# Kernel optimization log

Hardware: AMD Instinct MI355X
Metric: run time of the kernel (lower is better)

Reference implementation:

```python
import jax, jax.numpy as jnp
import numpy as np

ALPHA, GAMMA = 0.25, 2.0
CLASS_W, COORD_W, MASK_W = 2.0, 5.0, 5.0
EPS = 1e-8


def point_sample(masks, coords):
    """Bilinear sample (grid_sample, align_corners=False, zero padding).
    masks: [R, H, W]; coords: [P, 2] as (x, y) in [0, 1]. Returns [R, P]."""
    H, W = masks.shape[-2:]
    gx = 2.0 * coords[:, 0] - 1.0
    gy = 2.0 * coords[:, 1] - 1.0
    x = ((gx + 1.0) * W - 1.0) * 0.5
    y = ((gy + 1.0) * H - 1.0) * 0.5
    x0 = jnp.floor(x)
    y0 = jnp.floor(y)
    wx1 = x - x0
    wy1 = y - y0
    wx0 = 1.0 - wx1
    wy0 = 1.0 - wy1
    x0i = x0.astype(jnp.int32)
    y0i = y0.astype(jnp.int32)
    x1i = x0i + 1
    y1i = y0i + 1

    def gather(ix, iy):
        valid = ((ix >= 0) & (ix < W) & (iy >= 0) & (iy < H)).astype(masks.dtype)
        ixc = jnp.clip(ix, 0, W - 1)
        iyc = jnp.clip(iy, 0, H - 1)
        return masks[:, iyc, ixc] * valid  # [R, P]

    return (gather(x0i, y0i) * (wx0 * wy0)
            + gather(x1i, y0i) * (wx1 * wy0)
            + gather(x0i, y1i) * (wx0 * wy1)
            + gather(x1i, y1i) * (wx1 * wy1))


def setup_inputs() -> dict:
    key = jax.random.key(0)
    k1, k2, k3, k4, k5, k6 = jax.random.split(key, 6)
    bs, Q, n_ctrl, Hm, Wm, T, P = 8, 300, 16, 128, 128, 160, 12544
    return {
        "pred_logits": jax.random.normal(k1, (bs, Q, 1), jnp.float32),
        "pred_ctrl_points": jax.random.uniform(k2, (bs, Q, n_ctrl, 2), jnp.float32),
        "pred_seg_mask": jax.random.normal(k3, (bs, Q, Hm, Wm), jnp.float32),
        "tgt_pts": jax.random.uniform(k4, (T, n_ctrl, 2), jnp.float32),
        "tgt_masks": jax.random.uniform(k5, (T, Hm, Wm), jnp.float32),
        "point_coords": jax.random.uniform(k6, (P, 2), jnp.float32),
        "lvl": 0,
    }


def reference(pred_logits, pred_ctrl_points, pred_seg_mask, tgt_pts, tgt_masks, point_coords, lvl):
    bs, Q = pred_logits.shape[:2]
    out_prob = jax.nn.sigmoid(pred_logits.reshape(bs * Q, -1))          # [N, 1]
    out_pts = pred_ctrl_points.reshape(bs * Q, -1)                      # [N, 2*n_ctrl]
    tgt_flat = tgt_pts.reshape(tgt_pts.shape[0], -1)                    # [T, 2*n_ctrl]

    cost_mask_dice = 0.0
    if lvl < 2:  # num_seg_layers
        out_masks = pred_seg_mask.reshape(bs * Q, *pred_seg_mask.shape[-2:])
        # nearest-interp of tgt_masks to out_masks size is identity (same size)
        t_pts_samp = point_sample(tgt_masks, point_coords)              # [T, P]
        o_pts_samp = point_sample(out_masks, point_coords)              # [N, P]
        s = jax.nn.sigmoid(o_pts_samp)                                  # dice_loss sigmoids inputs
        numerator = 2.0 * jnp.einsum('np,tp->nt', s, t_pts_samp)        # [N, T]
        denominator = s.sum(-1)[:, None] + t_pts_samp.sum(-1)[None, :]
        cost_mask_dice = 1.0 - (numerator + 1.0) / (denominator + 1.0)

    neg_cost = (1.0 - ALPHA) * out_prob ** GAMMA * (-jnp.log(1.0 - out_prob + EPS))
    pos_cost = ALPHA * (1.0 - out_prob) ** GAMMA * (-jnp.log(out_prob + EPS))
    cost_class = pos_cost - neg_cost                                    # [N, 1]

    cost_kpts = jnp.abs(out_pts[:, None, :] - tgt_flat[None, :, :]).sum(-1)  # L1 cdist [N, T]

    C = CLASS_W * cost_class + COORD_W * cost_kpts + MASK_W * cost_mask_dice
    return C.reshape(bs, Q, -1)
```

## Files before the change

### kernel.cpp

```cpp
#include <hip/hip_runtime.h>
#include <hip/hip_bf16.h>
#include <cstdint>

#define HW 128
#define MASK_ELEMS (HW * HW)
#define SBLK 1024
#define NBLK 256

typedef unsigned short ushort_t;
typedef __attribute__((ext_vector_type(4))) unsigned short ushort4_t;
typedef __attribute__((ext_vector_type(8))) short short8;
typedef __attribute__((ext_vector_type(4))) float f32x4;

__device__ __forceinline__ float asf(unsigned int u) {
    union { unsigned int i; float f; } c;
    c.i = u;
    return c.f;
}
__device__ __forceinline__ ushort_t f2bf(float f) {
    union { float f; unsigned int i; } c;
    c.f = f;
    unsigned int r = c.i + 0x7FFFu + ((c.i >> 16) & 1u);
    return (ushort_t)(r >> 16);
}

__global__ void kprep(const float* __restrict__ coords, int* __restrict__ idx,
                      uint2* __restrict__ wpk, int P) {
    int i = blockIdx.x * 256 + threadIdx.x;
    if (i >= P) return;
    float cx = coords[2 * i], cy = coords[2 * i + 1];
    float x = cx * (float)HW - 0.5f;
    float y = cy * (float)HW - 0.5f;
    float x0f = floorf(x), y0f = floorf(y);
    float wx1 = x - x0f, wy1 = y - y0f;
    float wx0 = 1.f - wx1, wy0 = 1.f - wy1;
    int x0 = (int)x0f, y0 = (int)y0f;

    float wxA = (x0 >= 0) ? wx0 : wx1;
    float wxB = (x0 >= 0 && x0 < HW - 1) ? wx1 : 0.f;
    float wyA = (y0 >= 0) ? wy0 : wy1;
    float wyB = (y0 >= 0 && y0 < HW - 1) ? wy1 : 0.f;
    int bx = max(x0, 0), by = max(y0, 0);
    if (bx > HW - 2) { bx = HW - 2; wxB = wxA; wxA = 0.f; }
    if (by > HW - 2) { by = HW - 2; wyB = wyA; wyA = 0.f; }

    idx[i] = by * HW + bx;
    wpk[i] = make_uint2((unsigned)f2bf(wxA * wyA) | ((unsigned)f2bf(wxB * wyA) << 16),
                        (unsigned)f2bf(wxA * wyB) | ((unsigned)f2bf(wxB * wyB) << 16));
}

__device__ __forceinline__ void stage_mask(const float* __restrict__ g, float* l, int tid) {
    #pragma unroll
    for (int j = 0; j < MASK_ELEMS / (SBLK * 4); ++j) {
        int o = j * SBLK * 4 + tid * 4;
        __builtin_amdgcn_global_load_lds(
            (const __attribute__((address_space(1))) unsigned int*)(const void*)(g + o),
            (__attribute__((address_space(3))) unsigned int*)(void*)(l + o), 16, 0, 0);
    }
}

__global__ __launch_bounds__(SBLK) void ksamp_all(
        const float* __restrict__ pmask, const float* __restrict__ tmasks,
        const int* __restrict__ idx, const uint2* __restrict__ wpk,
        ushort_t* __restrict__ S, ushort_t* __restrict__ tsamp,
        float* __restrict__ ssum, float* __restrict__ tsum,
        const int* __restrict__ lvl, int N, int T, int P) {
    if (*lvl >= 2) return;
    __shared__ float buf[2][MASK_ELEMS];
    __shared__ float wred[2][SBLK / 64];
    __shared__ int4  tmi[64];
    __shared__ uint4 tma[64], tmb[64];
    const int tid = threadIdx.x;
    const int NM = N + T;
    const int nq = P >> 2;
    const int ntail = nq - 3 * SBLK;

    int4 idr[3];
    uint4 war[3], wbr[3];
    #pragma unroll
    for (int it = 0; it < 3; ++it) {
        int q = it * SBLK + tid;
        if (q < nq) {
            idr[it] = ((const int4*)idx)[q];
            war[it] = ((const uint4*)wpk)[2 * q];
            wbr[it] = ((const uint4*)wpk)[2 * q + 1];
        } else {
            idr[it] = make_int4(0, 0, 0, 0);
            war[it] = make_uint4(0, 0, 0, 0);
            wbr[it] = make_uint4(0, 0, 0, 0);
        }
    }

    auto mptr = [&](int mi) -> const float* {
        return (mi < N) ? pmask + (size_t)mi * MASK_ELEMS
                        : tmasks + (size_t)(mi - N) * MASK_ELEMS;
    };

    const int b = blockIdx.x;
    const int rounds = (NM - b + NBLK - 1) / NBLK;
    if (rounds <= 0) return;

    stage_mask(mptr(b), buf[0], tid);
    if (ntail > 0 && ntail <= 64 && tid < ntail) {
        int q = 3 * SBLK + tid;
        tmi[tid] = ((const int4*)idx)[q];
        tma[tid] = ((const uint4*)wpk)[2 * q];
        tmb[tid] = ((const uint4*)wpk)[2 * q + 1];
    }
    asm volatile("s_waitcnt vmcnt(0)" ::: "memory");
    asm volatile("s_waitcnt lgkmcnt(0)" ::: "memory");
    __builtin_amdgcn_s_barrier();

    int cur = 0;
    for (int k = 0; k < rounds; ++k) {
        if (k + 1 < rounds)
            stage_mask(mptr(b + (k + 1) * NBLK), buf[cur ^ 1], tid);

        const float* lm = buf[cur];
        const int mi = b + k * NBLK;
        const bool sig = (mi < N);
        ushort4_t* o4 = sig ? (ushort4_t*)(S + (size_t)mi * P)
                            : (ushort4_t*)(tsamp + (size_t)(mi - N) * P);
        float sum = 0.f;

        auto do_quad = [&](int4 id, uint4 wa4, uint4 wb4, int q) {
            float v[4];
            int bi[4] = {id.x, id.y, id.z, id.w};
            unsigned wa[4] = {wa4.x, wa4.z, wb4.x, wb4.z};
            unsigned wb[4] = {wa4.y, wa4.w, wb4.y, wb4.w};
            #pragma unroll
            for (int p2 = 0; p2 < 4; ++p2) {
                int bb = bi[p2];
                float t00 = lm[bb], t01 = lm[bb + 1];
                float t10 = lm[bb + HW], t11 = lm[bb + HW + 1];
                float vv = asf(wa[p2] << 16) * t00 + asf(wa[p2] & 0xffff0000u) * t01
                         + asf(wb[p2] << 16) * t10 + asf(wb[p2] & 0xffff0000u) * t11;
                if (sig) vv = __builtin_amdgcn_rcpf(1.f + __expf(-vv));
                v[p2] = vv;
            }
            ushort4_t o = {f2bf(v[0]), f2bf(v[1]), f2bf(v[2]), f2bf(v[3])};
            o4[q] = o;
            sum += (v[0] + v[1]) + (v[2] + v[3]);
        };

        #pragma unroll
        for (int it = 0; it < 3; ++it) {
            int q = it * SBLK + tid;
            if (q < nq) do_quad(idr[it], war[it], wbr[it], q);
        }
        if (ntail > 0 && ntail <= 64) {
            int tq = tid >> 4;
            if (((tid & 15) == 0) && tq < ntail)
                do_quad(tmi[tq], tma[tq], tmb[tq], 3 * SBLK + tq);
        } else if (ntail > 64) {
            for (int q = 3 * SBLK + tid; q < nq; q += SBLK)
                do_quad(((const int4*)idx)[q], ((const uint4*)wpk)[2 * q],
                        ((const uint4*)wpk)[2 * q + 1], q);
        }

        #pragma unroll
        for (int m2 = 32; m2 > 0; m2 >>= 1) sum += __shfl_xor(sum, m2, 64);
        if ((tid & 63) == 0) wred[k & 1][tid >> 6] = sum;
        asm volatile("s_waitcnt vmcnt(0)" ::: "memory");
        asm volatile("s_waitcnt lgkmcnt(0)" ::: "memory");
        __builtin_amdgcn_s_barrier();
        if (tid == 0) {
            float s = 0.f;
            #pragma unroll
            for (int w2 = 0; w2 < SBLK / 64; ++w2) s += wred[k & 1][w2];
            if (sig) ssum[mi] = s;
            else tsum[mi - N] = s;
        }
        cur ^= 1;
    }
}

#define LDF(Aarr, Barr, kof)                                                              \
    do {                                                                                  \
        _Pragma("unroll") for (int m_ = 0; m_ < 3; ++m_)                                  \
            Aarr[m_] = *(const short8*)(pa + (size_t)m_ * 16 * P + (kof));                \
        _Pragma("unroll") for (int j_ = 0; j_ < 5; ++j_)                                  \
            Barr[j_] = *(const short8*)(pb + (size_t)j_ * 16 * P + (kof));                \
    } while (0)

#define FMAS(Aarr, Barr)                                                                  \
    do {                                                                                  \
        _Pragma("unroll") for (int m_ = 0; m_ < 3; ++m_) {                                \
            _Pragma("unroll") for (int j_ = 0; j_ < 5; ++j_)                              \
                acc[m_][j_] = __builtin_amdgcn_mfma_f32_16x16x32_bf16(                    \
                    Aarr[m_], Barr[j_], acc[m_][j_], 0, 0, 0);                            \
        }                                                                                 \
    } while (0)

__global__ __launch_bounds__(256) void kgemm(const ushort_t* __restrict__ S,
                                             const ushort_t* __restrict__ Tm,
                                             float* __restrict__ Cpart,
                                             const int* __restrict__ lvl,
                                             int N, int T, int P, int nsteps) {
    if (*lvl >= 2) return;
    int tid = threadIdx.x;
    int wid = tid >> 6, lane = tid & 63;
    int wm = wid >> 1, wt = wid & 1;
    int r = lane & 15, g = lane >> 4;
    int n0 = blockIdx.x * 96 + wm * 48;
    int t0 = wt * 80;
    size_t k0 = (size_t)blockIdx.y * nsteps * 32 + g * 8;
    const ushort_t* pa = S + (size_t)(n0 + r) * P + k0;
    const ushort_t* pb = Tm + (size_t)(t0 + r) * P + k0;

    f32x4 acc[3][5];
    #pragma unroll
    for (int m2 = 0; m2 < 3; ++m2)
        #pragma unroll
        for (int j2 = 0; j2 < 5; ++j2) acc[m2][j2] = (f32x4){0.f, 0.f, 0.f, 0.f};

    short8 a0[3], b0[5], a1[3], b1[5];
    LDF(a0, b0, 0);
    int ks = 0;
    for (; ks + 2 < nsteps; ks += 2) {
        LDF(a1, b1, (ks + 1) * 32);
        FMAS(a0, b0);
        LDF(a0, b0, (ks + 2) * 32);
        FMAS(a1, b1);
    }
    LDF(a1, b1, (ks + 1) * 32);
    FMAS(a0, b0);
    FMAS(a1, b1);

    size_t cb = (size_t)blockIdx.y * N * T;
    #pragma unroll
    for (int m2 = 0; m2 < 3; ++m2)
        #pragma unroll
        for (int j2 = 0; j2 < 5; ++j2)
            #pragma unroll
            for (int q = 0; q < 4; ++q) {
                int row = n0 + m2 * 16 + g * 4 + q;
                int col = t0 + j2 * 16 + r;
                Cpart[cb + (size_t)row * T + col] = acc[m2][j2][q];
            }
}

__global__ void kfinal(const float* __restrict__ logits, const float* __restrict__ opts,
                       const float* __restrict__ tpts, const float* __restrict__ Cpart,
                       const float* __restrict__ ssum, const float* __restrict__ tsum,
                       const int* __restrict__ lvl, float* __restrict__ out,
                       int N, int T, int nks) {
    int idx = blockIdx.x * 256 + threadIdx.x;
    if (idx >= N * T) return;
    int n = idx / T, t = idx - n * T;

    float lg = logits[n];
    float p = 1.f / (1.f + __expf(-lg));
    float pos = 0.25f * (1.f - p) * (1.f - p) * (-logf(p + 1e-8f));
    float neg = 0.75f * p * p * (-logf(1.f - p + 1e-8f));
    float ccls = pos - neg;

    float kp = 0.f;
    const float4* a4 = (const float4*)(opts + (size_t)n * 32);
    const float4* b4 = (const float4*)(tpts + (size_t)t * 32);
    #pragma unroll
    for (int j = 0; j < 8; ++j) {
        float4 a = a4[j], b = b4[j];
        kp += fabsf(a.x - b.x) + fabsf(a.y - b.y) + fabsf(a.z - b.z) + fabsf(a.w - b.w);
    }

    float dice = 0.f;
    if (*lvl < 2) {
        float dot = 0.f;
        for (int ks = 0; ks < nks; ++ks) dot += Cpart[(size_t)ks * N * T + idx];
        dice = 1.f - (2.f * dot + 1.f) / (ssum[n] + tsum[t] + 1.f);
    }
    out[idx] = 2.f * ccls + 5.f * kp + 5.f * dice;
}

extern "C" void kernel_launch(void* const* d_in, const int* in_sizes, int n_in,
                              void* d_out, int out_size, void* d_ws, size_t ws_size,
                              hipStream_t stream) {
    const float* logits = (const float*)d_in[0];
    const float* cpts   = (const float*)d_in[1];
    const float* pmask  = (const float*)d_in[2];
    const float* tpts   = (const float*)d_in[3];
    const float* tmasks = (const float*)d_in[4];
    const float* coords = (const float*)d_in[5];
    const int*   lvl    = (const int*)d_in[6];
    float* out = (float*)d_out;

    int N = in_sizes[0];
    int T = in_sizes[3] / 32;
    int P = in_sizes[5] / 2;

    char* w = (char*)d_ws;
    auto alloc = [&](size_t bytes) {
        char* r = w;
        w += (bytes + 255) & ~(size_t)255;
        return r;
    };
    int*      idxb  = (int*)alloc((size_t)P * 4);
    uint2*    wpkb  = (uint2*)alloc((size_t)P * 8);
    ushort_t* tsamp = (ushort_t*)alloc((size_t)T * P * 2);
    ushort_t* S     = (ushort_t*)alloc((size_t)N * P * 2);
    float*    ssumb = (float*)alloc((size_t)N * 4);
    float*    tsumb = (float*)alloc((size_t)T * 4);
    size_t base_bytes = (size_t)(w - (char*)d_ws);

    int nks = 14;
    if (base_bytes + (size_t)nks * N * T * 4 > ws_size) nks = 7;
    int nsteps = (P / 32) / nks;
    float* Cpart = (float*)alloc((size_t)nks * N * T * 4);

    kprep<<<(P + 255) / 256, 256, 0, stream>>>(coords, idxb, wpkb, P);
    ksamp_all<<<NBLK, SBLK, 0, stream>>>(pmask, tmasks, idxb, wpkb, S, tsamp,
                                         ssumb, tsumb, lvl, N, T, P);
    kgemm<<<dim3(N / 96, nks), 256, 0, stream>>>(S, tsamp, Cpart, lvl, N, T, P, nsteps);
    kfinal<<<(N * T + 255) / 256, 256, 0, stream>>>(logits, cpts, tpts, Cpart, ssumb, tsumb,
                                                    lvl, out, N, T, nks);
}
```

Measured before the change: 129.8 us.

## Warp-specialize sampling kernel into loader and sampler waves with LDS flag sync

Splits the 1024-thread block into 4 producer waves that copy each mask from global into a double-buffered LDS slot via registers, and 12 consumer waves that bilinear-sample it. The two groups synchronize through LDS atomic counters with spin-waits instead of block-wide barriers. The aim is to overlap mask staging with sampling and remove per-round full barriers. In exchange it drops the async global_load_lds path and the register-cached indices/weights, reloading them every round. Spin-waiting also consumes issue slots and carries hang risk, bounded only by a guard counter.

```diff
diff --git a/kernel.cpp b/kernel.cpp
--- a/kernel.cpp
+++ b/kernel.cpp
@@ -6,6 +6,10 @@
 #define MASK_ELEMS (HW * HW)
 #define SBLK 1024
 #define NBLK 256
+#define NSW 12
+#define NLW 4
+#define STH (NSW * 64)
+#define LTH (NLW * 64)
 
 typedef unsigned short ushort_t;
 typedef __attribute__((ext_vector_type(4))) unsigned short ushort4_t;
@@ -22,6 +26,15 @@
     c.f = f;
     unsigned int r = c.i + 0x7FFFu + ((c.i >> 16) & 1u);
     return (ushort_t)(r >> 16);
+}
+
+__device__ __forceinline__ void spin_ge(int* p, int target) {
+    int guard = 0;
+    while (__hip_atomic_load(p, __ATOMIC_ACQUIRE, __HIP_MEMORY_SCOPE_WORKGROUP) < target) {
+        __builtin_amdgcn_s_sleep(1);
+        if (++guard > (1 << 28)) break;
+    }
+    __builtin_amdgcn_sched_barrier(0);
 }
 
 __global__ void kprep(const float* __restrict__ coords, int* __restrict__ idx,
@@ -49,16 +62,6 @@
                         (unsigned)f2bf(wxA * wyB) | ((unsigned)f2bf(wxB * wyB) << 16));
 }
 
-__device__ __forceinline__ void stage_mask(const float* __restrict__ g, float* l, int tid) {
-    #pragma unroll
-    for (int j = 0; j < MASK_ELEMS / (SBLK * 4); ++j) {
-        int o = j * SBLK * 4 + tid * 4;
-        __builtin_amdgcn_global_load_lds(
-            (const __attribute__((address_space(1))) unsigned int*)(const void*)(g + o),
-            (__attribute__((address_space(3))) unsigned int*)(void*)(l + o), 16, 0, 0);
-    }
-}
-
 __global__ __launch_bounds__(SBLK) void ksamp_all(
         const float* __restrict__ pmask, const float* __restrict__ tmasks,
         const int* __restrict__ idx, const uint2* __restrict__ wpk,
@@ -67,111 +70,105 @@
         const int* __restrict__ lvl, int N, int T, int P) {
     if (*lvl >= 2) return;
     __shared__ float buf[2][MASK_ELEMS];
-    __shared__ float wred[2][SBLK / 64];
-    __shared__ int4  tmi[64];
-    __shared__ uint4 tma[64], tmb[64];
+    __shared__ float wred[4][NSW];
+    __shared__ int part_cnt, cons_cnt;
     const int tid = threadIdx.x;
+    const int wid = tid >> 6, lane = tid & 63;
     const int NM = N + T;
     const int nq = P >> 2;
-    const int ntail = nq - 3 * SBLK;
-
-    int4 idr[3];
-    uint4 war[3], wbr[3];
-    #pragma unroll
-    for (int it = 0; it < 3; ++it) {
-        int q = it * SBLK + tid;
-        if (q < nq) {
-            idr[it] = ((const int4*)idx)[q];
-            war[it] = ((const uint4*)wpk)[2 * q];
-            wbr[it] = ((const uint4*)wpk)[2 * q + 1];
-        } else {
-            idr[it] = make_int4(0, 0, 0, 0);
-            war[it] = make_uint4(0, 0, 0, 0);
-            wbr[it] = make_uint4(0, 0, 0, 0);
-        }
-    }
+
+    if (tid == 0) { part_cnt = 0; cons_cnt = 0; }
+    __syncthreads();
+
+    const int b = blockIdx.x;
+    const int rounds = (NM - b + NBLK - 1) / NBLK;
+    if (rounds <= 0) return;
 
     auto mptr = [&](int mi) -> const float* {
         return (mi < N) ? pmask + (size_t)mi * MASK_ELEMS
                         : tmasks + (size_t)(mi - N) * MASK_ELEMS;
     };
 
-    const int b = blockIdx.x;
-    const int rounds = (NM - b + NBLK - 1) / NBLK;
-    if (rounds <= 0) return;
-
-    stage_mask(mptr(b), buf[0], tid);
-    if (ntail > 0 && ntail <= 64 && tid < ntail) {
-        int q = 3 * SBLK + tid;
-        tmi[tid] = ((const int4*)idx)[q];
-        tma[tid] = ((const uint4*)wpk)[2 * q];
-        tmb[tid] = ((const uint4*)wpk)[2 * q + 1];
-    }
-    asm volatile("s_waitcnt vmcnt(0)" ::: "memory");
-    asm volatile("s_waitcnt lgkmcnt(0)" ::: "memory");
-    __builtin_amdgcn_s_barrier();
-
-    int cur = 0;
-    for (int k = 0; k < rounds; ++k) {
-        if (k + 1 < rounds)
-            stage_mask(mptr(b + (k + 1) * NBLK), buf[cur ^ 1], tid);
-
-        const float* lm = buf[cur];
-        const int mi = b + k * NBLK;
-        const bool sig = (mi < N);
-        ushort4_t* o4 = sig ? (ushort4_t*)(S + (size_t)mi * P)
-                            : (ushort4_t*)(tsamp + (size_t)(mi - N) * P);
-        float sum = 0.f;
-
-        auto do_quad = [&](int4 id, uint4 wa4, uint4 wb4, int q) {
-            float v[4];
-            int bi[4] = {id.x, id.y, id.z, id.w};
-            unsigned wa[4] = {wa4.x, wa4.z, wb4.x, wb4.z};
-            unsigned wb[4] = {wa4.y, wa4.w, wb4.y, wb4.w};
-            #pragma unroll
-            for (int p2 = 0; p2 < 4; ++p2) {
-                int bb = bi[p2];
-                float t00 = lm[bb], t01 = lm[bb + 1];
-                float t10 = lm[bb + HW], t11 = lm[bb + HW + 1];
-                float vv = asf(wa[p2] << 16) * t00 + asf(wa[p2] & 0xffff0000u) * t01
-                         + asf(wb[p2] << 16) * t10 + asf(wb[p2] & 0xffff0000u) * t11;
-                if (sig) vv = __builtin_amdgcn_rcpf(1.f + __expf(-vv));
-                v[p2] = vv;
+    if (wid >= NSW) {
+        const int lt = tid - STH;
+        for (int k = 0; k < rounds; ++k) {
+            if (k >= 2) spin_ge(&cons_cnt, NSW * (k - 1));
+            const float4* g4 = (const float4*)mptr(b + k * NBLK);
+            float4* b4 = (float4*)buf[k & 1];
+            float4 v[8];
+            #pragma unroll
+            for (int j = 0; j < 8; ++j) v[j] = g4[lt + LTH * j];
+            #pragma unroll
+            for (int j = 0; j < 8; ++j) {
+                b4[lt + LTH * j] = v[j];
+                v[j] = g4[lt + LTH * (8 + j)];
             }
-            ushort4_t o = {f2bf(v[0]), f2bf(v[1]), f2bf(v[2]), f2bf(v[3])};
-            o4[q] = o;
-            sum += (v[0] + v[1]) + (v[2] + v[3]);
-        };
-
-        #pragma unroll
-        for (int it = 0; it < 3; ++it) {
-            int q = it * SBLK + tid;
-            if (q < nq) do_quad(idr[it], war[it], wbr[it], q);
+            #pragma unroll
+            for (int j = 0; j < 8; ++j) b4[lt + LTH * (8 + j)] = v[j];
+            asm volatile("s_waitcnt lgkmcnt(0)" ::: "memory");
+            if (lane == 0) atomicAdd(&part_cnt, 1);
         }
-        if (ntail > 0 && ntail <= 64) {
-            int tq = tid >> 4;
-            if (((tid & 15) == 0) && tq < ntail)
-                do_quad(tmi[tq], tma[tq], tmb[tq], 3 * SBLK + tq);
-        } else if (ntail > 64) {
-            for (int q = 3 * SBLK + tid; q < nq; q += SBLK)
-                do_quad(((const int4*)idx)[q], ((const uint4*)wpk)[2 * q],
-                        ((const uint4*)wpk)[2 * q + 1], q);
+    } else {
+        const int st = tid;
+        const int4* idx4 = (const int4*)idx;
+        const uint4* w4 = (const uint4*)wpk;
+        for (int k = 0; k < rounds; ++k) {
+            spin_ge(&part_cnt, NLW * (k + 1));
+            const float* lm = buf[k & 1];
+            const int mi = b + k * NBLK;
+            const bool sig = (mi < N);
+            ushort4_t* o4 = sig ? (ushort4_t*)(S + (size_t)mi * P)
+                                : (ushort4_t*)(tsamp + (size_t)(mi - N) * P);
+            float sum = 0.f;
+
+            int q = st;
+            int4 id = idx4[q];
+            uint4 wa = w4[2 * q], wb = w4[2 * q + 1];
+            #pragma unroll
+            for (int j = 0; j < 5; ++j) {
+                int qn = q + STH;
+                bool hn = (j < 4) && (qn < nq);
+                int4 idn;
+                uint4 wan, wbn;
+                if (hn) { idn = idx4[qn]; wan = w4[2 * qn]; wbn = w4[2 * qn + 1]; }
+
+                float v[4];
+                int bi[4] = {id.x, id.y, id.z, id.w};
+                unsigned ua[4] = {wa.x, wa.z, wb.x, wb.z};
+                unsigned ub[4] = {wa.y, wa.w, wb.y, wb.w};
+                #pragma unroll
+                for (int p2 = 0; p2 < 4; ++p2) {
+                    int bb = bi[p2];
+                    float t00 = lm[bb], t01 = lm[bb + 1];
+                    float t10 = lm[bb + HW], t11 = lm[bb + HW + 1];
+                    float vv = asf(ua[p2] << 16) * t00 + asf(ua[p2] & 0xffff0000u) * t01
+                             + asf(ub[p2] << 16) * t10 + asf(ub[p2] & 0xffff0000u) * t11;
+                    if (sig) vv = __builtin_amdgcn_rcpf(1.f + __expf(-vv));
+                    v[p2] = vv;
+                }
+                ushort4_t o = {f2bf(v[0]), f2bf(v[1]), f2bf(v[2]), f2bf(v[3])};
+                o4[q] = o;
+                sum += (v[0] + v[1]) + (v[2] + v[3]);
+
+                if (!hn) break;
+                q = qn;
+                id = idn; wa = wan; wb = wbn;
+            }
+
+            #pragma unroll
+            for (int m2 = 32; m2 > 0; m2 >>= 1) sum += __shfl_xor(sum, m2, 64);
+            if (lane == 0) wred[k & 3][wid] = sum;
+            asm volatile("s_waitcnt lgkmcnt(0)" ::: "memory");
+            if (lane == 0) atomicAdd(&cons_cnt, 1);
+            if (wid == 0 && lane == 0) {
+                spin_ge(&cons_cnt, NSW * (k + 1));
+                float s = 0.f;
+                #pragma unroll
+                for (int w2 = 0; w2 < NSW; ++w2) s += wred[k & 3][w2];
+                if (sig) ssum[mi] = s;
+                else tsum[mi - N] = s;
+            }
         }
-
-        #pragma unroll
-        for (int m2 = 32; m2 > 0; m2 >>= 1) sum += __shfl_xor(sum, m2, 64);
-        if ((tid & 63) == 0) wred[k & 1][tid >> 6] = sum;
-        asm volatile("s_waitcnt vmcnt(0)" ::: "memory");
-        asm volatile("s_waitcnt lgkmcnt(0)" ::: "memory");
-        __builtin_amdgcn_s_barrier();
-        if (tid == 0) {
-            float s = 0.f;
-            #pragma unroll
-            for (int w2 = 0; w2 < SBLK / 64; ++w2) s += wred[k & 1][w2];
-            if (sig) ssum[mi] = s;
-            else tsum[mi - N] = s;
-        }
-        cur ^= 1;
     }
 }
 
```

Result: slower. 152.5 us (+17.5%).
